# Kernel tuning notes

Measured on AMD Instinct MI355X. Metric: run time of the kernel, lower is better.

The kernel has to match this reference:

```python
import jax, jax.numpy as jnp
import numpy as np

N = 100000
E = 1600000
IN_CH = 64
HID = 128
OUT_CH = 16
N_LAYERS = 3
N_CLUSTERS = 4
NUM_GRAPHS = 64
BN_EPS = 1e-5


def setup_inputs() -> dict:
    key = jax.random.key(0)
    ks = jax.random.split(key, 16)
    x = jax.random.normal(ks[0], (N, IN_CH), jnp.float32)
    cluster = jax.random.randint(ks[1], (N,), 0, N_CLUSTERS, jnp.int32)
    edge_index = jax.random.randint(ks[2], (2, E), 0, N, jnp.int32)
    batch = jnp.sort(jax.random.randint(ks[3], (N,), 0, NUM_GRAPHS, jnp.int32))
    # per-(layer, cluster) GCNConv params
    W0 = jax.random.normal(ks[4], (N_CLUSTERS, IN_CH, HID), jnp.float32) * 0.05
    b0 = jnp.zeros((N_CLUSTERS, HID), jnp.float32)
    Wh = jax.random.normal(ks[5], (N_LAYERS - 1, N_CLUSTERS, HID, HID), jnp.float32) * 0.05
    bh = jnp.zeros((N_LAYERS - 1, N_CLUSTERS, HID), jnp.float32)
    # pool MLP: [HID*N_LAYERS, HID, OUT_CH], batch_norm + relu on hidden layer
    mlp_W1 = jax.random.normal(ks[6], (HID * N_LAYERS, HID), jnp.float32) * 0.05
    mlp_b1 = jnp.zeros((HID,), jnp.float32)
    bn_gamma = jnp.ones((HID,), jnp.float32)
    bn_beta = jnp.zeros((HID,), jnp.float32)
    mlp_W2 = jax.random.normal(ks[7], (HID, OUT_CH), jnp.float32) * 0.05
    mlp_b2 = jnp.zeros((OUT_CH,), jnp.float32)
    return dict(x=x, cluster=cluster, edge_index=edge_index, batch=batch,
                W0=W0, b0=b0, Wh=Wh, bh=bh,
                mlp_W1=mlp_W1, mlp_b1=mlp_b1, bn_gamma=bn_gamma, bn_beta=bn_beta,
                mlp_W2=mlp_W2, mlp_b2=mlp_b2)


def _forward(x, cluster, edge_index, batch, W0, b0, Wh, bh,
             mlp_W1, mlp_b1, bn_gamma, bn_beta, mlp_W2, mlp_b2):
    n = x.shape[0]
    self_loop = jnp.arange(n, dtype=edge_index.dtype)
    row = jnp.concatenate([edge_index[0], self_loop])  # source
    col = jnp.concatenate([edge_index[1], self_loop])  # target
    # gcn_norm: deg over targets (incl. self loops), sym normalization
    deg = jax.ops.segment_sum(jnp.ones(row.shape, x.dtype), col, num_segments=n)
    dinv = jnp.where(deg > 0, jax.lax.rsqrt(deg), 0.0)
    enorm = dinv[row] * dinv[col]  # [E+N]

    def prop(h):  # scatter-add aggregation: out[col] += norm * h[row]
        return jax.ops.segment_sum(enorm[:, None] * h[row], col, num_segments=n)

    h = x
    pools = []
    for t in range(N_LAYERS):
        x2 = jnp.zeros((n, HID), x.dtype)
        for c in range(N_CLUSTERS):
            W = W0[c] if t == 0 else Wh[t - 1, c]
            b = b0[c] if t == 0 else bh[t - 1, c]
            out_c = prop(h @ W) + b  # full-graph GCNConv for cluster c
            x2 = jnp.where((cluster == c)[:, None], out_c, x2)  # keep masked rows
        h = x2
        pools.append(jax.ops.segment_sum(h, batch, num_segments=NUM_GRAPHS))
    z = jnp.concatenate(pools, axis=1)  # [G, HID*L]
    z = z @ mlp_W1 + mlp_b1
    mu = jnp.mean(z, axis=0)
    var = jnp.mean(jnp.square(z - mu), axis=0)
    z = (z - mu) * jax.lax.rsqrt(var + BN_EPS) * bn_gamma + bn_beta
    z = jax.nn.relu(z)
    return z @ mlp_W2 + mlp_b2


def reference(x, cluster, edge_index, batch, W0, b0, Wh, bh,
              mlp_W1, mlp_b1, bn_gamma, bn_beta, mlp_W2, mlp_b2):
    return _forward(x, cluster, edge_index, batch, W0, b0, Wh, bh,
                    mlp_W1, mlp_b1, bn_gamma, bn_beta, mlp_W2, mlp_b2)
```

## Files before the change

### kernel.cpp

```cpp
#include <hip/hip_runtime.h>
#include <hip/hip_fp16.h>

#define HID 128
#define NCLUST 4
#define NGRAPH 64
#define NLAYERS 3
#define NBMAX 512
#define SCAP 5120
#define BIN_CHUNK 8192

typedef _Float16 f16x8 __attribute__((ext_vector_type(8)));
typedef float f32x4 __attribute__((ext_vector_type(4)));

__global__ __launch_bounds__(256) void k_setup(const float* __restrict__ x,
                                               __half* __restrict__ x16, int nxf,
                                               const float* __restrict__ W0,
                                               __half* __restrict__ W0T,
                                               const float* __restrict__ Wh,
                                               __half* __restrict__ WhT,
                                               float* __restrict__ pool,
                                               int* __restrict__ cc,
                                               int* __restrict__ bcur) {
    long i = (long)blockIdx.x * 256 + threadIdx.x;
    const int P = NLAYERS * NGRAPH * HID;
    if (i < P) { pool[i] = 0.f; return; }
    i -= P;
    if (i < 12) { cc[i] = 0; return; }
    i -= 12;
    if (i < NBMAX) { bcur[i] = (int)i * SCAP; return; }
    i -= NBMAX;
    long nx4 = nxf / 4;
    if (i < nx4) {
        long idx = i * 4;
        float4 v = *(const float4*)(x + idx);
        __half2* dst = (__half2*)(x16 + idx);
        dst[0] = __floats2half2_rn(v.x, v.y);
        dst[1] = __floats2half2_rn(v.z, v.w);
        return;
    }
    i -= nx4;
    if (i < NCLUST * 128 * 64) {
        int m = (int)(i >> 13);
        int rem = (int)(i & 8191);
        int o = rem >> 6, k = rem & 63;
        W0T[i] = __float2half(W0[(size_t)m * 8192 + (size_t)k * 128 + o]);
        return;
    }
    i -= NCLUST * 128 * 64;
    if (i < 2 * NCLUST * 128 * 128) {
        int m = (int)(i >> 14);
        int rem = (int)(i & 16383);
        int o = rem >> 7, k = rem & 127;
        WhT[i] = __float2half(Wh[(size_t)m * 16384 + (size_t)k * 128 + o]);
        return;
    }
}

__global__ __launch_bounds__(256) void k_bin(const int* __restrict__ ei,
                                             int* __restrict__ bcur,
                                             unsigned int* __restrict__ stage, int E) {
    __shared__ int hcnt[NBMAX];
    __shared__ int hbase[NBMAX];
    int t = threadIdx.x;
    int start = blockIdx.x * BIN_CHUNK;
    int end = min(start + BIN_CHUNK, E);
    for (int b = t; b < NBMAX; b += 256) hcnt[b] = 0;
    __syncthreads();
    for (int i = start + t; i < end; i += 256)
        atomicAdd(&hcnt[ei[E + i] >> 8], 1);
    __syncthreads();
    for (int b = t; b < NBMAX; b += 256) {
        hbase[b] = hcnt[b] ? atomicAdd(&bcur[b], hcnt[b]) : 0;
        hcnt[b] = 0;
    }
    __syncthreads();
    for (int i = start + t; i < end; i += 256) {
        int c = ei[E + i];
        int b = c >> 8;
        int r = atomicAdd(&hcnt[b], 1);
        stage[hbase[b] + r] = ((unsigned int)(c & 255) << 24) | (unsigned int)ei[i];
    }
}

__global__ __launch_bounds__(256) void k_csrify(const unsigned int* __restrict__ stage,
                                                const int* __restrict__ bcur,
                                                int* __restrict__ esrc,
                                                int* __restrict__ offs,
                                                int* __restrict__ deg,
                                                float* __restrict__ dinv,
                                                const int* __restrict__ cluster,
                                                int* __restrict__ ccur,
                                                int* __restrict__ clist, int n) {
    __shared__ int sh[256];
    __shared__ int lofs[256];
    __shared__ int lsrc[SCAP];
    __shared__ int lcc[NCLUST];
    __shared__ int lcb[NCLUST];
    int b = blockIdx.x, t = threadIdx.x;
    int base = b * SCAP;
    int cnt = bcur[b] - base;
    int node = b * 256 + t;
    sh[t] = 0;
    if (t < NCLUST) lcc[t] = 0;
    __syncthreads();
    for (int j = t; j < cnt; j += 256)
        atomicAdd(&sh[stage[base + j] >> 24], 1);
    int c = -1, lp = 0;
    if (node < n) { c = cluster[node]; lp = atomicAdd(&lcc[c], 1); }
    __syncthreads();
    int v0 = sh[t];
    if (t < NCLUST) lcb[t] = lcc[t] ? atomicAdd(&ccur[t], lcc[t]) : 0;
    __syncthreads();
    for (int d = 1; d < 256; d <<= 1) {
        int v = (t >= d) ? sh[t - d] : 0;
        __syncthreads();
        sh[t] += v;
        __syncthreads();
    }
    lofs[t] = sh[t] - v0;
    if (node < n) {
        offs[node] = base + lofs[t];
        deg[node] = v0;
        dinv[node] = rsqrtf((float)(v0 + 1));
        clist[(size_t)c * n + lcb[c] + lp] = node;
    }
    __syncthreads();
    for (int j = t; j < cnt; j += 256) {
        unsigned int e = stage[base + j];
        int r = atomicAdd(&lofs[e >> 24], 1);
        lsrc[r] = (int)(e & 0xFFFFFFu);
    }
    __syncthreads();
    for (int j = t; j < cnt; j += 256) esrc[base + j] = lsrc[j];
}

__global__ __launch_bounds__(256) void k_agg64(const __half* __restrict__ hin,
                                               const int* __restrict__ offs,
                                               const int* __restrict__ deg,
                                               const int* __restrict__ esrc,
                                               const float* __restrict__ dinv,
                                               __half* __restrict__ out, int n) {
    int node = __builtin_amdgcn_readfirstlane(
        (int)((blockIdx.x * blockDim.x + threadIdx.x) >> 6));
    if (node >= n) return;
    int lane = threadIdx.x & 63;
    int s = offs[node], e = s + deg[node];
    const __half* hp = hin + lane;
    float a0 = 0.f;
    int j = s;
    for (; j + 15 < e; j += 16) {
        int idx[16];
        {
            int4 qa = *(const int4*)(esrc + j);
            int4 qb = *(const int4*)(esrc + j + 4);
            int4 qc = *(const int4*)(esrc + j + 8);
            int4 qd = *(const int4*)(esrc + j + 12);
            idx[0] = qa.x; idx[1] = qa.y; idx[2] = qa.z; idx[3] = qa.w;
            idx[4] = qb.x; idx[5] = qb.y; idx[6] = qb.z; idx[7] = qb.w;
            idx[8] = qc.x; idx[9] = qc.y; idx[10] = qc.z; idx[11] = qc.w;
            idx[12] = qd.x; idx[13] = qd.y; idx[14] = qd.z; idx[15] = qd.w;
        }
        float w[16];
        __half r[16];
#pragma unroll
        for (int p = 0; p < 16; ++p) {
            w[p] = dinv[idx[p]];
            r[p] = hp[(size_t)idx[p] * 64];
        }
#pragma unroll
        for (int p = 0; p < 16; ++p) a0 = fmaf(w[p], __half2float(r[p]), a0);
    }
    for (; j + 3 < e; j += 4) {
        int4 s4 = *(const int4*)(esrc + j);
        float w0 = dinv[s4.x];
        float w1 = dinv[s4.y];
        float w2 = dinv[s4.z];
        float w3 = dinv[s4.w];
        float v0 = __half2float(hp[(size_t)s4.x * 64]);
        float v1 = __half2float(hp[(size_t)s4.y * 64]);
        float v2 = __half2float(hp[(size_t)s4.z * 64]);
        float v3 = __half2float(hp[(size_t)s4.w * 64]);
        a0 = fmaf(w0, v0, a0);
        a0 = fmaf(w1, v1, a0);
        a0 = fmaf(w2, v2, a0);
        a0 = fmaf(w3, v3, a0);
    }
    for (; j < e; ++j) {
        int src = esrc[j];
        a0 = fmaf(dinv[src], __half2float(hp[(size_t)src * 64]), a0);
    }
    float dm = dinv[node];
    a0 = dm * fmaf(dm, __half2float(hp[(size_t)node * 64]), a0);
    out[(size_t)node * 64 + lane] = __float2half(a0);
}

__global__ __launch_bounds__(256) void k_agg128(const __half* __restrict__ hin,
                                                const int* __restrict__ offs,
                                                const int* __restrict__ deg,
                                                const int* __restrict__ esrc,
                                                const float* __restrict__ dinv,
                                                __half* __restrict__ out, int n) {
    int node = __builtin_amdgcn_readfirstlane(
        (int)((blockIdx.x * blockDim.x + threadIdx.x) >> 6));
    if (node >= n) return;
    int lane = threadIdx.x & 63;
    int s = offs[node], e = s + deg[node];
    const __half2* hp = (const __half2*)hin + lane;
    float a0 = 0.f, a1 = 0.f;
    int j = s;
    for (; j + 15 < e; j += 16) {
        int idx[16];
        {
            int4 qa = *(const int4*)(esrc + j);
            int4 qb = *(const int4*)(esrc + j + 4);
            int4 qc = *(const int4*)(esrc + j + 8);
            int4 qd = *(const int4*)(esrc + j + 12);
            idx[0] = qa.x; idx[1] = qa.y; idx[2] = qa.z; idx[3] = qa.w;
            idx[4] = qb.x; idx[5] = qb.y; idx[6] = qb.z; idx[7] = qb.w;
            idx[8] = qc.x; idx[9] = qc.y; idx[10] = qc.z; idx[11] = qc.w;
            idx[12] = qd.x; idx[13] = qd.y; idx[14] = qd.z; idx[15] = qd.w;
        }
        float w[16];
        __half2 r[16];
#pragma unroll
        for (int p = 0; p < 16; ++p) {
            w[p] = dinv[idx[p]];
            r[p] = hp[(size_t)idx[p] * 64];
        }
#pragma unroll
        for (int p = 0; p < 16; ++p) {
            float2 f = __half22float2(r[p]);
            a0 = fmaf(w[p], f.x, a0);
            a1 = fmaf(w[p], f.y, a1);
        }
    }
    for (; j + 3 < e; j += 4) {
        int4 s4 = *(const int4*)(esrc + j);
        float w0 = dinv[s4.x];
        float w1 = dinv[s4.y];
        float w2 = dinv[s4.z];
        float w3 = dinv[s4.w];
        float2 v0 = __half22float2(hp[(size_t)s4.x * 64]);
        float2 v1 = __half22float2(hp[(size_t)s4.y * 64]);
        float2 v2 = __half22float2(hp[(size_t)s4.z * 64]);
        float2 v3 = __half22float2(hp[(size_t)s4.w * 64]);
        a0 = fmaf(w0, v0.x, a0); a1 = fmaf(w0, v0.y, a1);
        a0 = fmaf(w1, v1.x, a0); a1 = fmaf(w1, v1.y, a1);
        a0 = fmaf(w2, v2.x, a0); a1 = fmaf(w2, v2.y, a1);
        a0 = fmaf(w3, v3.x, a0); a1 = fmaf(w3, v3.y, a1);
    }
    for (; j < e; ++j) {
        int src = esrc[j];
        float w = dinv[src];
        float2 v = __half22float2(hp[(size_t)src * 64]);
        a0 = fmaf(w, v.x, a0); a1 = fmaf(w, v.y, a1);
    }
    float dm = dinv[node];
    float2 vs = __half22float2(hp[(size_t)node * 64]);
    a0 = dm * fmaf(dm, vs.x, a0);
    a1 = dm * fmaf(dm, vs.y, a1);
    ((__half2*)out)[(size_t)node * 64 + lane] = __floats2half2_rn(a0, a1);
}

template <int K>
__global__ __launch_bounds__(256) void k_tf(const __half* __restrict__ agg16,
                                            const __half* __restrict__ WT,
                                            const float* __restrict__ ball,
                                            const int* __restrict__ ccur,
                                            const int* __restrict__ clist,
                                            const int* __restrict__ batch,
                                            float* __restrict__ pool,
                                            __half* __restrict__ hout, int n) {
    __shared__ int idxs[64];
    __shared__ int gb[64];
    __shared__ __half ot[64][136];
    int c = blockIdx.y;
    int cnt = ccur[c];
    int m0 = blockIdx.x * 64;
    if (m0 >= cnt) return;
    size_t base = (size_t)c * n;
    int tid = threadIdx.x;
    if (tid < 64) {
        int mm = m0 + tid;
        int id = (mm < cnt) ? clist[base + mm] : -1;
        idxs[tid] = id;
        gb[tid] = (id >= 0) ? batch[id] : -1;
    }
    __syncthreads();
    int w = tid >> 6, l = tid & 63;
    int lr = l & 15, lg = l >> 4;
    int arow = idxs[w * 16 + lr];
    int arow_s = arow < 0 ? 0 : arow;
    const __half* Ap = agg16 + (size_t)arow_s * K + lg * 8;
    const __half* Bp = WT + (size_t)c * 128 * K + (size_t)lr * K + lg * 8;
    f32x4 acc[8];
#pragma unroll
    for (int ct = 0; ct < 8; ++ct) acc[ct] = (f32x4){0.f, 0.f, 0.f, 0.f};
#pragma unroll
    for (int k0 = 0; k0 < K; k0 += 32) {
        f16x8 a = *(const f16x8*)(Ap + k0);
#pragma unroll
        for (int ct = 0; ct < 8; ++ct) {
            f16x8 b = *(const f16x8*)(Bp + (size_t)ct * 16 * K + k0);
            acc[ct] = __builtin_amdgcn_mfma_f32_16x16x32_f16(a, b, acc[ct], 0, 0, 0);
        }
    }
#pragma unroll
    for (int ct = 0; ct < 8; ++ct) {
        float bz = ball[c * 128 + ct * 16 + lr];
#pragma unroll
        for (int r = 0; r < 4; ++r) {
            int nl = w * 16 + lg * 4 + r;
            ot[nl][ct * 16 + lr] = __float2half(acc[ct][r] + bz);
        }
    }
    __syncthreads();
    for (int idx = tid; idx < 64 * 16; idx += 256) {
        int nl = idx >> 4, seg = idx & 15;
        int node = idxs[nl];
        if (node >= 0) {
            float4 v = *(const float4*)&ot[nl][seg * 8];
            *(float4*)(hout + (size_t)node * 128 + seg * 8) = v;
        }
    }
    if (tid < 128) {
        float acc2 = 0.f;
        int cur = -1;
        for (int r = 0; r < 64; ++r) {
            int g = gb[r];
            if (g < 0) break;
            if (g != cur) {
                if (cur >= 0) atomicAdd(&pool[cur * HID + tid], acc2);
                acc2 = 0.f;
                cur = g;
            }
            acc2 += __half2float(ot[r][tid]);
        }
        if (cur >= 0) atomicAdd(&pool[cur * HID + tid], acc2);
    }
}

__global__ __launch_bounds__(128) void k_mlp1(const float* __restrict__ pool,
                                              const float* __restrict__ W1,
                                              const float* __restrict__ b1,
                                              float* __restrict__ z1) {
    int g = blockIdx.x, j = threadIdx.x;
    float acc = b1[j];
#pragma unroll 8
    for (int k = 0; k < NLAYERS * HID; ++k) {
        int t = k >> 7, jj = k & 127;
        float a = pool[((size_t)t * NGRAPH + g) * HID + jj];
        acc += a * W1[(size_t)k * HID + j];
    }
    z1[g * HID + j] = acc;
}

__global__ __launch_bounds__(256) void k_mlp2(const float* __restrict__ z1,
                                              const float* __restrict__ gamma,
                                              const float* __restrict__ beta,
                                              const float* __restrict__ W2,
                                              const float* __restrict__ b2,
                                              float* __restrict__ out) {
    __shared__ float Z[NGRAPH * HID];
    __shared__ float Zn[NGRAPH * HID];
    for (int idx = threadIdx.x; idx < NGRAPH * HID; idx += 256) Z[idx] = z1[idx];
    __syncthreads();
    if (threadIdx.x < HID) {
        int j = threadIdx.x;
        float mu = 0.f;
        for (int g = 0; g < NGRAPH; ++g) mu += Z[g * HID + j];
        mu *= (1.f / NGRAPH);
        float var = 0.f;
        for (int g = 0; g < NGRAPH; ++g) {
            float d = Z[g * HID + j] - mu;
            var += d * d;
        }
        var *= (1.f / NGRAPH);
        float inv = rsqrtf(var + 1e-5f) * gamma[j];
        float bb = beta[j];
        for (int g = 0; g < NGRAPH; ++g) {
            float v = (Z[g * HID + j] - mu) * inv + bb;
            Zn[g * HID + j] = v > 0.f ? v : 0.f;
        }
    }
    __syncthreads();
    for (int idx = threadIdx.x; idx < NGRAPH * 16; idx += 256) {
        int g = idx >> 4, o = idx & 15;
        float acc = b2[o];
#pragma unroll 16
        for (int j = 0; j < HID; ++j) acc += Zn[g * HID + j] * W2[j * 16 + o];
        out[idx] = acc;
    }
}

extern "C" void kernel_launch(void* const* d_in, const int* in_sizes, int n_in,
                              void* d_out, int out_size, void* d_ws, size_t ws_size,
                              hipStream_t stream) {
    const float* x       = (const float*)d_in[0];
    const int*   cluster = (const int*)d_in[1];
    const int*   ei      = (const int*)d_in[2];
    const int*   batch   = (const int*)d_in[3];
    const float* W0      = (const float*)d_in[4];
    const float* b0      = (const float*)d_in[5];
    const float* Wh      = (const float*)d_in[6];
    const float* bh      = (const float*)d_in[7];
    const float* W1      = (const float*)d_in[8];
    const float* b1      = (const float*)d_in[9];
    const float* gamma   = (const float*)d_in[10];
    const float* beta    = (const float*)d_in[11];
    const float* W2      = (const float*)d_in[12];
    const float* b2      = (const float*)d_in[13];

    const int n  = in_sizes[1];
    const int E  = in_sizes[2] / 2;
    const int IN = in_sizes[0] / n;
    float* out = (float*)d_out;

    const int nbuck = (n + 255) / 256;

    char* ws = (char*)d_ws;
    size_t off = 0;
    auto alloc = [&](size_t b) { size_t o = off; off += (b + 255) & ~(size_t)255; return o; };
    int*    deg    = (int*)(ws + alloc((size_t)n * 4));
    int*    offs   = (int*)(ws + alloc((size_t)n * 4));
    float*  dinv   = (float*)(ws + alloc((size_t)n * 4));
    int*    esrc   = (int*)(ws + alloc((size_t)nbuck * SCAP * 4));
    unsigned int* stage = (unsigned int*)(ws + alloc((size_t)nbuck * SCAP * 4));
    int*    bcur   = (int*)(ws + alloc((size_t)NBMAX * 4));
    int*    cc     = (int*)(ws + alloc(12 * 4));
    int*    clist  = (int*)(ws + alloc((size_t)NCLUST * n * 4));
    __half* x16    = (__half*)(ws + alloc((size_t)n * IN * 2));
    __half* agg16  = (__half*)(ws + alloc((size_t)n * HID * 2));
    __half* hbuf   = (__half*)(ws + alloc((size_t)n * HID * 2));
    __half* W0T    = (__half*)(ws + alloc((size_t)NCLUST * 128 * 64 * 2));
    __half* WhT    = (__half*)(ws + alloc((size_t)2 * NCLUST * 128 * 128 * 2));
    float*  pool   = (float*)(ws + alloc((size_t)NLAYERS * NGRAPH * HID * 4));
    float*  z1     = (float*)(ws + alloc((size_t)NGRAPH * HID * 4));
    int* ccur = cc + 8;

    long setup_items = (long)NLAYERS * NGRAPH * HID + 12 + NBMAX +
                       (long)n * IN / 4 + NCLUST * 128 * 64 + 2 * NCLUST * 128 * 128;
    int setup_blocks = (int)((setup_items + 255) / 256);
    hipLaunchKernelGGL(k_setup, dim3(setup_blocks), dim3(256), 0, stream,
                       x, x16, n * IN, W0, W0T, Wh, WhT, pool, cc, bcur);
    hipLaunchKernelGGL(k_bin, dim3((E + BIN_CHUNK - 1) / BIN_CHUNK), dim3(256), 0, stream,
                       ei, bcur, stage, E);
    hipLaunchKernelGGL(k_csrify, dim3(nbuck), dim3(256), 0, stream,
                       stage, bcur, esrc, offs, deg, dinv, cluster, ccur, clist, n);

    dim3 tgrid((n + 63) / 64, NCLUST);
    int aggblocks = (n + 3) / 4;

    hipLaunchKernelGGL(k_agg64, dim3(aggblocks), dim3(256), 0, stream,
                       x16, offs, deg, esrc, dinv, agg16, n);
    hipLaunchKernelGGL(k_tf<64>, tgrid, dim3(256), 0, stream,
                       agg16, W0T, b0, ccur, clist, batch,
                       pool + 0 * NGRAPH * HID, hbuf, n);

    for (int t = 1; t < NLAYERS; ++t) {
        hipLaunchKernelGGL(k_agg128, dim3(aggblocks), dim3(256), 0, stream,
                           hbuf, offs, deg, esrc, dinv, agg16, n);
        hipLaunchKernelGGL(k_tf<128>, tgrid, dim3(256), 0, stream,
                           agg16, WhT + (size_t)(t - 1) * NCLUST * 128 * 128,
                           bh + (size_t)(t - 1) * NCLUST * HID,
                           ccur, clist, batch, pool + (size_t)t * NGRAPH * HID, hbuf, n);
    }

    hipLaunchKernelGGL(k_mlp1, dim3(NGRAPH), dim3(128), 0, stream, pool, W1, b1, z1);
    hipLaunchKernelGGL(k_mlp2, dim3(1), dim3(256), 0, stream, z1, gamma, beta, W2, b2, out);

    (void)n_in; (void)out_size; (void)ws_size;
}
```

Before: 384.1 us.

## Cache bin keys in LDS, widen csrify blocks, stage GEMM rows in shared memory

k_bin now uses smaller chunks and keeps each edge's bucket and low byte in shared memory, so the second pass does not reload the target indices from global memory. k_csrify runs with 512 threads, with the extra threads only helping in the edge loops. k_tf first gathers each block's 64 aggregated rows into a shared buffer with coalesced row loads, then feeds the MFMA A operand from LDS instead of doing strided global loads per lane, and reuses that buffer for output staging. This adds shared-memory traffic and an extra barrier, and the smaller bin chunks mean more atomic increments on the global bucket counters.

```diff
diff --git a/kernel.cpp b/kernel.cpp
--- a/kernel.cpp
+++ b/kernel.cpp
@@ -7,7 +7,7 @@
 #define NLAYERS 3
 #define NBMAX 512
 #define SCAP 5120
-#define BIN_CHUNK 8192
+#define BIN_CHUNK 2048
 
 typedef _Float16 f16x8 __attribute__((ext_vector_type(8)));
 typedef float f32x4 __attribute__((ext_vector_type(4)));
@@ -61,28 +61,34 @@
                                              unsigned int* __restrict__ stage, int E) {
     __shared__ int hcnt[NBMAX];
     __shared__ int hbase[NBMAX];
+    __shared__ unsigned short lb[BIN_CHUNK];
+    __shared__ unsigned char llo[BIN_CHUNK];
     int t = threadIdx.x;
     int start = blockIdx.x * BIN_CHUNK;
     int end = min(start + BIN_CHUNK, E);
+    int m = end - start;
     for (int b = t; b < NBMAX; b += 256) hcnt[b] = 0;
     __syncthreads();
-    for (int i = start + t; i < end; i += 256)
-        atomicAdd(&hcnt[ei[E + i] >> 8], 1);
+    for (int i = t; i < m; i += 256) {
+        int col = ei[E + start + i];
+        lb[i] = (unsigned short)(col >> 8);
+        llo[i] = (unsigned char)(col & 255);
+        atomicAdd(&hcnt[col >> 8], 1);
+    }
     __syncthreads();
     for (int b = t; b < NBMAX; b += 256) {
         hbase[b] = hcnt[b] ? atomicAdd(&bcur[b], hcnt[b]) : 0;
         hcnt[b] = 0;
     }
     __syncthreads();
-    for (int i = start + t; i < end; i += 256) {
-        int c = ei[E + i];
-        int b = c >> 8;
+    for (int i = t; i < m; i += 256) {
+        int b = lb[i];
         int r = atomicAdd(&hcnt[b], 1);
-        stage[hbase[b] + r] = ((unsigned int)(c & 255) << 24) | (unsigned int)ei[i];
-    }
-}
-
-__global__ __launch_bounds__(256) void k_csrify(const unsigned int* __restrict__ stage,
+        stage[hbase[b] + r] = ((unsigned int)llo[i] << 24) | (unsigned int)ei[start + i];
+    }
+}
+
+__global__ __launch_bounds__(512) void k_csrify(const unsigned int* __restrict__ stage,
                                                 const int* __restrict__ bcur,
                                                 int* __restrict__ esrc,
                                                 int* __restrict__ offs,
@@ -100,38 +106,38 @@
     int base = b * SCAP;
     int cnt = bcur[b] - base;
     int node = b * 256 + t;
-    sh[t] = 0;
+    if (t < 256) sh[t] = 0;
     if (t < NCLUST) lcc[t] = 0;
     __syncthreads();
-    for (int j = t; j < cnt; j += 256)
+    for (int j = t; j < cnt; j += 512)
         atomicAdd(&sh[stage[base + j] >> 24], 1);
     int c = -1, lp = 0;
-    if (node < n) { c = cluster[node]; lp = atomicAdd(&lcc[c], 1); }
-    __syncthreads();
-    int v0 = sh[t];
+    if (t < 256 && node < n) { c = cluster[node]; lp = atomicAdd(&lcc[c], 1); }
+    __syncthreads();
+    int v0 = (t < 256) ? sh[t] : 0;
     if (t < NCLUST) lcb[t] = lcc[t] ? atomicAdd(&ccur[t], lcc[t]) : 0;
     __syncthreads();
     for (int d = 1; d < 256; d <<= 1) {
-        int v = (t >= d) ? sh[t - d] : 0;
+        int v = (t >= d && t < 256) ? sh[t - d] : 0;
         __syncthreads();
-        sh[t] += v;
+        if (t < 256) sh[t] += v;
         __syncthreads();
     }
-    lofs[t] = sh[t] - v0;
-    if (node < n) {
+    if (t < 256) lofs[t] = sh[t] - v0;
+    if (t < 256 && node < n) {
         offs[node] = base + lofs[t];
         deg[node] = v0;
         dinv[node] = rsqrtf((float)(v0 + 1));
         clist[(size_t)c * n + lcb[c] + lp] = node;
     }
     __syncthreads();
-    for (int j = t; j < cnt; j += 256) {
+    for (int j = t; j < cnt; j += 512) {
         unsigned int e = stage[base + j];
         int r = atomicAdd(&lofs[e >> 24], 1);
         lsrc[r] = (int)(e & 0xFFFFFFu);
     }
     __syncthreads();
-    for (int j = t; j < cnt; j += 256) esrc[base + j] = lsrc[j];
+    for (int j = t; j < cnt; j += 512) esrc[base + j] = lsrc[j];
 }
 
 __global__ __launch_bounds__(256) void k_agg64(const __half* __restrict__ hin,
@@ -273,7 +279,7 @@
                                             __half* __restrict__ hout, int n) {
     __shared__ int idxs[64];
     __shared__ int gb[64];
-    __shared__ __half ot[64][136];
+    __shared__ __half buf[64][136];
     int c = blockIdx.y;
     int cnt = ccur[c];
     int m0 = blockIdx.x * 64;
@@ -288,30 +294,40 @@
     }
     __syncthreads();
     int w = tid >> 6, l = tid & 63;
+#pragma unroll
+    for (int r = 0; r < 16; ++r) {
+        int row = idxs[w * 16 + r];
+        int rs = row < 0 ? 0 : row;
+        if constexpr (K == 128) {
+            __half2 v = ((const __half2*)(agg16 + (size_t)rs * K))[l];
+            *((__half2*)&buf[w * 16 + r][0] + l) = v;
+        } else {
+            buf[w * 16 + r][l] = agg16[(size_t)rs * K + l];
+        }
+    }
+    __syncthreads();
     int lr = l & 15, lg = l >> 4;
-    int arow = idxs[w * 16 + lr];
-    int arow_s = arow < 0 ? 0 : arow;
-    const __half* Ap = agg16 + (size_t)arow_s * K + lg * 8;
     const __half* Bp = WT + (size_t)c * 128 * K + (size_t)lr * K + lg * 8;
     f32x4 acc[8];
 #pragma unroll
     for (int ct = 0; ct < 8; ++ct) acc[ct] = (f32x4){0.f, 0.f, 0.f, 0.f};
 #pragma unroll
     for (int k0 = 0; k0 < K; k0 += 32) {
-        f16x8 a = *(const f16x8*)(Ap + k0);
+        f16x8 a = *(const f16x8*)&buf[w * 16 + lr][lg * 8 + k0];
 #pragma unroll
         for (int ct = 0; ct < 8; ++ct) {
             f16x8 b = *(const f16x8*)(Bp + (size_t)ct * 16 * K + k0);
             acc[ct] = __builtin_amdgcn_mfma_f32_16x16x32_f16(a, b, acc[ct], 0, 0, 0);
         }
     }
+    __syncthreads();
 #pragma unroll
     for (int ct = 0; ct < 8; ++ct) {
         float bz = ball[c * 128 + ct * 16 + lr];
 #pragma unroll
         for (int r = 0; r < 4; ++r) {
             int nl = w * 16 + lg * 4 + r;
-            ot[nl][ct * 16 + lr] = __float2half(acc[ct][r] + bz);
+            buf[nl][ct * 16 + lr] = __float2half(acc[ct][r] + bz);
         }
     }
     __syncthreads();
@@ -319,7 +335,7 @@
         int nl = idx >> 4, seg = idx & 15;
         int node = idxs[nl];
         if (node >= 0) {
-            float4 v = *(const float4*)&ot[nl][seg * 8];
+            float4 v = *(const float4*)&buf[nl][seg * 8];
             *(float4*)(hout + (size_t)node * 128 + seg * 8) = v;
         }
     }
@@ -334,7 +350,7 @@
                 acc2 = 0.f;
                 cur = g;
             }
-            acc2 += __half2float(ot[r][tid]);
+            acc2 += __half2float(buf[r][tid]);
         }
         if (cur >= 0) atomicAdd(&pool[cur * HID + tid], acc2);
     }
@@ -445,7 +461,7 @@
                        x, x16, n * IN, W0, W0T, Wh, WhT, pool, cc, bcur);
     hipLaunchKernelGGL(k_bin, dim3((E + BIN_CHUNK - 1) / BIN_CHUNK), dim3(256), 0, stream,
                        ei, bcur, stage, E);
-    hipLaunchKernelGGL(k_csrify, dim3(nbuck), dim3(256), 0, stream,
+    hipLaunchKernelGGL(k_csrify, dim3(nbuck), dim3(512), 0, stream,
                        stage, bcur, esrc, offs, deg, dinv, cluster, ccur, clist, n);
 
     dim3 tgrid((n + 63) / 64, NCLUST);
```

New measurement: 378.3 us. About the same (-1.5%).
